# Kernel tuning notes

Hardware: AMD Instinct MI355X
Metric: run time of the kernel (lower is better)

The kernel has to match this reference:

```python
import jax, jax.numpy as jnp
import numpy as np

B, K, C, H, W = 16, 512, 512, 64, 64

def setup_inputs() -> dict:
    key = jax.random.key(0)
    kx, kc = jax.random.split(key)
    x = jax.random.normal(kx, (B, C, H, W), dtype=jnp.float32)
    cluster_centers = jax.random.normal(kc, (1, K, C, 1, 1), dtype=jnp.float32)
    return {"x": x, "cluster_centers": cluster_centers}

def reference(x, cluster_centers):
    # Faithful to: torch.square(x[:, None] - centers).sum(2).argmin(1, keepdim=True)
    # Computed without the (B, K, C, H, W) broadcast intermediate via
    # and numerically the same distances up to fp rounding).
    c = cluster_centers[0, :, :, 0, 0]                      # (K, C)
    x_sq = jnp.sum(x * x, axis=1, keepdims=True)            # (B, 1, H, W)
    c_sq = jnp.sum(c * c, axis=1)[None, :, None, None]      # (1, K, 1, 1)
    cross = jnp.einsum('bchw,kc->bkhw', x, c)               # (B, K, H, W)
    dist = x_sq - 2.0 * cross + c_sq                        # (B, K, H, W)
    return jnp.argmin(dist, axis=1, keepdims=True)          # (B, 1, H, W) int
```

## Files before the change

### kernel.cpp

```cpp
#include <hip/hip_runtime.h>
#include <math.h>


#define NK   512
#define NC   512
#define NHW  4096
#define NPX  65536
#define MARGIN 0.05f

typedef unsigned short u16;
typedef __attribute__((ext_vector_type(8)))  _Float16 half8;
typedef __attribute__((ext_vector_type(8)))  unsigned short ushort8;
typedef __attribute__((ext_vector_type(16))) float  f32x16;

__device__ __forceinline__ u16 f2h(float f) {
    return __builtin_bit_cast(u16, (_Float16)f);
}

__global__ __launch_bounds__(64) void prep_pack(const float* __restrict__ cc,
                                                u16* __restrict__ wcc,
                                                float* __restrict__ shalf,
                                                double* __restrict__ csqd,
                                                float* __restrict__ cct) {
    const int k    = blockIdx.x;
    const int lane = threadIdx.x;
    const int c0   = lane * 8;
    const float* row = cc + (size_t)k * NC + c0;
    ushort8 hi;
    double dsum = 0.0;
    #pragma unroll
    for (int i = 0; i < 8; ++i) {
        float v = row[i];
        dsum = fma((double)v, (double)v, dsum);
        hi[i] = f2h(v);
        cct[(size_t)(c0 + i) * NK + k] = v;
    }
    const int ch  = c0 >> 4;
    const int kh  = (c0 >> 3) & 1;
    const int mtg = k >> 5;
    const int h   = mtg >> 3;
    const int mtl = mtg & 7;
    const int ls  = (k & 31) + 32 * kh;
    *(ushort8*)(wcc + (((size_t)(ch * 2 + h) * 8 + mtl) * 64 + ls) * 8) = hi;
    #pragma unroll
    for (int off = 32; off > 0; off >>= 1) dsum += __shfl_down(dsum, off, 64);
    if (lane == 0) {
        csqd[k]  = dsum;
        shalf[k] = 0.5f * (float)dsum;
    }
}

__global__ __launch_bounds__(256, 4) void codebook_mfma(
        const float* __restrict__ x,
        const u16* __restrict__ wcc,
        const float* __restrict__ shalf,
        float* __restrict__ cbv,
        float* __restrict__ csv,
        int*   __restrict__ ckk)
{
    __shared__ __align__(16) u16 cs0[16 * 512];
    __shared__ __align__(16) u16 cs1[16 * 512];
    __shared__ __align__(16) u16 xs0[4 * 512];
    __shared__ __align__(16) u16 xs1[4 * 512];

    const int tid  = threadIdx.x;
    const int w    = tid >> 6;
    const int lane = tid & 63;

    const int h   = blockIdx.x & 1;
    const int gp0 = (blockIdx.x >> 1) * 64;
    const float* xb = x + (size_t)(gp0 >> 12) * (NC * NHW) + (gp0 & (NHW - 1));

    f32x16 acc[2][2] = {};

    const int p   = tid & 63;
    const int xkh = w & 1;
    const int jq  = w >> 1;
    const int xoff = ((p >> 5) * 64 + ((p & 31) + 32 * xkh)) * 8 + jq * 4;
    const float* xp = xb + (size_t)(xkh * 8 + jq * 4) * NHW + p;

    float fxa[8], fxb[8];

    auto xload = [&](float* fx, int sc) {
        const float* xc0 = xp + (size_t)(2 * sc) * 16 * NHW;
        const float* xc1 = xc0 + 16 * NHW;
        fx[0] = xc0[0]; fx[1] = xc0[NHW]; fx[2] = xc0[2 * NHW]; fx[3] = xc0[3 * NHW];
        fx[4] = xc1[0]; fx[5] = xc1[NHW]; fx[6] = xc1[2 * NHW]; fx[7] = xc1[3 * NHW];
    };
    auto xwrite = [&](const float* fx, u16* xs) {
        #pragma unroll
        for (int sub = 0; sub < 2; ++sub) {
            u16 h0 = f2h(fx[sub * 4 + 0]), h1 = f2h(fx[sub * 4 + 1]);
            u16 h2 = f2h(fx[sub * 4 + 2]), h3 = f2h(fx[sub * 4 + 3]);
            uint2 hv = make_uint2((unsigned)h0 | ((unsigned)h1 << 16),
                                  (unsigned)h2 | ((unsigned)h3 << 16));
            *(uint2*)&xs[sub * 1024 + xoff] = hv;
        }
    };
    auto stage_cs = [&](int sc, u16* dst) {
        #pragma unroll
        for (int sub = 0; sub < 2; ++sub) {
            #pragma unroll
            for (int i = 0; i < 2; ++i) {
                const int u = w * 2 + i;
                const u16* g = wcc + ((((size_t)(2 * sc + sub) * 2 + h) * 8 + u) * 64 + lane) * 8;
                __builtin_amdgcn_global_load_lds(
                    (const __attribute__((address_space(1))) void*)g,
                    (__attribute__((address_space(3))) void*)(dst + (sub * 8 + u) * 512),
                    16, 0, 0);
            }
        }
    };
    auto compute = [&](const u16* csb, const u16* xsb) {
        __builtin_amdgcn_s_setprio(1);
        #pragma unroll
        for (int sub = 0; sub < 2; ++sub) {
            half8 bh[2];
            #pragma unroll
            for (int nt = 0; nt < 2; ++nt)
                bh[nt] = *(const half8*)&xsb[sub * 1024 + ((size_t)nt * 64 + lane) * 8];
            #pragma unroll
            for (int mtl2 = 0; mtl2 < 2; ++mtl2) {
                const int gm = w * 2 + mtl2;
                half8 ah = *(const half8*)&csb[((size_t)(sub * 8 + gm) * 64 + lane) * 8];
                #pragma unroll
                for (int nt = 0; nt < 2; ++nt)
                    acc[mtl2][nt] = __builtin_amdgcn_mfma_f32_32x32x16_f16(ah, bh[nt], acc[mtl2][nt], 0, 0, 0);
            }
        }
        __builtin_amdgcn_s_setprio(0);
    };

    auto phase = [&](int t, u16* cs_cur, u16* cs_nxt, u16* xs_cur, u16* xs_nxt,
                     float* fx_cur, float* fx_nxt) {
        stage_cs(t + 1, cs_nxt);
        __builtin_amdgcn_sched_barrier(0);
        xload(fx_nxt, t + 2);
        asm volatile("s_waitcnt vmcnt(12)" ::: "memory");
        xwrite(fx_cur, xs_nxt);
        compute(cs_cur, xs_cur);
        asm volatile("s_waitcnt vmcnt(8) lgkmcnt(0)" ::: "memory");
        __builtin_amdgcn_s_barrier();
        __builtin_amdgcn_sched_barrier(0);
    };

    xload(fxa, 0);
    __builtin_amdgcn_sched_barrier(0);
    stage_cs(0, cs0);
    __builtin_amdgcn_sched_barrier(0);
    xload(fxb, 1);
    asm volatile("s_waitcnt vmcnt(12)" ::: "memory");
    xwrite(fxa, xs0);
    asm volatile("s_waitcnt vmcnt(8) lgkmcnt(0)" ::: "memory");
    __builtin_amdgcn_s_barrier();
    __builtin_amdgcn_sched_barrier(0);

    for (int t = 0; t < 14; t += 2) {
        phase(t,     cs0, cs1, xs0, xs1, fxb, fxa);
        phase(t + 1, cs1, cs0, xs1, xs0, fxa, fxb);
    }

    stage_cs(15, cs1);
    asm volatile("s_waitcnt vmcnt(4)" ::: "memory");
    xwrite(fxb, xs1);
    compute(cs0, xs0);
    asm volatile("s_waitcnt vmcnt(0) lgkmcnt(0)" ::: "memory");
    __builtin_amdgcn_s_barrier();
    __builtin_amdgcn_sched_barrier(0);
    compute(cs1, xs1);
    __syncthreads();

    float* cand_v = (float*)cs0;
    float* cand_s = cand_v + 512;
    int*   cand_k = (int*)(cand_s + 512);
    float* sh_ep  = (float*)(cand_k + 512);

    sh_ep[tid] = shalf[h * 256 + tid];
    __syncthreads();

    const int qb = lane >> 5;
    #pragma unroll
    for (int nt = 0; nt < 2; ++nt) {
        float best = -INFINITY, sec = -INFINITY;
        int bk = 0;
        #pragma unroll
        for (int mtl2 = 0; mtl2 < 2; ++mtl2) {
            const int kbase = w * 64 + mtl2 * 32 + 4 * qb;
            #pragma unroll
            for (int reg = 0; reg < 16; ++reg) {
                const int k = kbase + (reg & 3) + 8 * (reg >> 2);
                const float v = acc[mtl2][nt][reg] - sh_ep[k];
                if (v > best) { sec = best; best = v; bk = k; }
                else if (v > sec) sec = v;
            }
        }
        const int pc   = nt * 32 + (lane & 31);
        const int slot = w * 2 + qb;
        cand_v[pc * 8 + slot] = best;
        cand_s[pc * 8 + slot] = sec;
        cand_k[pc * 8 + slot] = bk;
    }
    __syncthreads();

    if (tid < 64) {
        float best = -INFINITY, sec = -INFINITY;
        int bk = 1 << 30;
        #pragma unroll
        for (int s = 0; s < 8; ++s) {
            float v  = cand_v[tid * 8 + s];
            float v2 = cand_s[tid * 8 + s];
            int  kk  = cand_k[tid * 8 + s];
            if (v > best || (v == best && kk < bk)) {
                sec = fmaxf(sec, best);
                best = v; bk = kk;
            } else sec = fmaxf(sec, v);
            sec = fmaxf(sec, v2);
        }
        const int gpx = gp0 + tid;
        cbv[h * NPX + gpx] = best;
        csv[h * NPX + gpx] = sec;
        ckk[h * NPX + gpx] = h * 256 + bk;
    }
}

__global__ __launch_bounds__(256) void merge_recheck(
        const float* __restrict__ x,
        const float* __restrict__ cct,
        const double* __restrict__ csqd,
        const float* __restrict__ cbv,
        const float* __restrict__ csv,
        const int*   __restrict__ ckk,
        int* __restrict__ out)
{
    __shared__ float  xcol[2][NC];
    __shared__ double part[2][4][NK];
    __shared__ double dvv[256];
    __shared__ int    dii[256];
    __shared__ int    list[64];
    __shared__ int    nflag;

    const int tid  = threadIdx.x;
    const int w    = tid >> 6;
    const int lane = tid & 63;
    const int pb   = blockIdx.x * 64;

    if (tid == 0) nflag = 0;
    __syncthreads();

    if (tid < 64) {
        const int px = pb + tid;
        const float b0 = cbv[px], b1 = cbv[NPX + px];
        const float s0 = csv[px], s1 = csv[NPX + px];
        const int   k0 = ckk[px], k1 = ckk[NPX + px];
        float best, sec; int bk;
        if (b0 >= b1) { best = b0; bk = k0; sec = fmaxf(s0, b1); }
        else          { best = b1; bk = k1; sec = fmaxf(s1, b0); }
        out[px] = bk;
        if (best - sec < MARGIN) { int i = atomicAdd(&nflag, 1); list[i] = px; }
    }
    __syncthreads();

    const int n = nflag;
    for (int idx = 0; idx < n; idx += 2) {
        const int px0 = list[idx];
        const int px1 = (idx + 1 < n) ? list[idx + 1] : px0;

        #pragma unroll
        for (int r = 0; r < 2; ++r) {
            const int c = tid + r * 256;
            xcol[0][c] = x[(size_t)(px0 >> 12) * (NC * NHW) + (size_t)c * NHW + (px0 & (NHW - 1))];
            xcol[1][c] = x[(size_t)(px1 >> 12) * (NC * NHW) + (size_t)c * NHW + (px1 & (NHW - 1))];
        }
        __syncthreads();

        double a0[8] = {}, a1[8] = {};
        const float4* cr = (const float4*)(cct + (size_t)(w * 128) * NK) + lane * 2;
        #pragma unroll 4
        for (int c0 = 0; c0 < 128; ++c0) {
            const float4 va = cr[0];
            const float4 vb = cr[1];
            cr += NK / 4;
            const double x0 = (double)xcol[0][w * 128 + c0];
            const double x1 = (double)xcol[1][w * 128 + c0];
            const double c4[8] = {(double)va.x, (double)va.y, (double)va.z, (double)va.w,
                                  (double)vb.x, (double)vb.y, (double)vb.z, (double)vb.w};
            #pragma unroll
            for (int j = 0; j < 8; ++j) {
                a0[j] = fma(x0, c4[j], a0[j]);
                a1[j] = fma(x1, c4[j], a1[j]);
            }
        }
        #pragma unroll
        for (int j = 0; j < 8; ++j) {
            part[0][w][lane * 8 + j] = a0[j];
            part[1][w][lane * 8 + j] = a1[j];
        }
        __syncthreads();

        #pragma unroll
        for (int pxi = 0; pxi < 2; ++pxi) {
            double bd = 1e300;
            int bkk = 1 << 30;
            #pragma unroll
            for (int r = 0; r < 2; ++r) {
                const int k = tid + r * 256;
                const double cross = part[pxi][0][k] + part[pxi][1][k]
                                   + part[pxi][2][k] + part[pxi][3][k];
                const double d = fma(-2.0, cross, csqd[k]);
                if (d < bd || (d == bd && k < bkk)) { bd = d; bkk = k; }
            }
            dvv[tid] = bd; dii[tid] = bkk;
            __syncthreads();
            for (int srd = 128; srd > 0; srd >>= 1) {
                if (tid < srd) {
                    double ov = dvv[tid + srd]; int oi = dii[tid + srd];
                    if (ov < dvv[tid] || (ov == dvv[tid] && oi < dii[tid])) {
                        dvv[tid] = ov; dii[tid] = oi;
                    }
                }
                __syncthreads();
            }
            if (tid == 0) out[pxi == 0 ? px0 : px1] = dii[0];
            __syncthreads();
        }
    }
}

extern "C" void kernel_launch(void* const* d_in, const int* in_sizes, int n_in,
                              void* d_out, int out_size, void* d_ws, size_t ws_size,
                              hipStream_t stream) {
    const float* x  = (const float*)d_in[0];
    const float* cc = (const float*)d_in[1];
    int* out = (int*)d_out;

    double* csqd  = (double*)d_ws;
    float*  shalf = (float*)(csqd + NK);
    u16*    wcc   = (u16*)(shalf + NK);
    float*  cct   = (float*)(wcc + 32 * 2 * 8 * 64 * 8);
    float*  cbv   = cct + (size_t)NC * NK;
    float*  csv   = cbv + 2 * NPX;
    int*    ckk   = (int*)(csv + 2 * NPX);

    prep_pack<<<NK, 64, 0, stream>>>(cc, wcc, shalf, csqd, cct);
    codebook_mfma<<<(NPX / 64) * 2, 256, 0, stream>>>(x, wcc, shalf, cbv, csv, ckk);
    merge_recheck<<<NPX / 64, 256, 0, stream>>>(x, cct, csqd, cbv, csv, ckk, out);
}
```

Before: 265.0 us.

## Split recheck into global-list fp32 pass with fp64 fallback for near-ties

Replaces the per-block merge+fp64 recheck with a global compaction of ambiguous pixels, a load-balanced fp32 recheck handling four pixels per pass, and an fp64 recheck only for pixels whose fp32 top-two gap is below a tight gate. This is meant to cut the expensive fp64 work and remove the load imbalance of per-block variable-length recheck loops. It adds two extra launches and global atomics, and it relies on the fp32 gate being tight enough to preserve exact argmin agreement.

Result: faster. 250.9 us (-5.3%).

```diff
diff --git a/kernel.cpp b/kernel.cpp
--- a/kernel.cpp
+++ b/kernel.cpp
@@ -7,6 +7,7 @@
 #define NHW  4096
 #define NPX  65536
 #define MARGIN 0.05f
+#define GATE2  1e-3f
 
 typedef unsigned short u16;
 typedef __attribute__((ext_vector_type(8)))  _Float16 half8;
@@ -21,9 +22,13 @@
                                                 u16* __restrict__ wcc,
                                                 float* __restrict__ shalf,
                                                 double* __restrict__ csqd,
-                                                float* __restrict__ cct) {
+                                                float* __restrict__ csqf,
+                                                float* __restrict__ cct,
+                                                int* __restrict__ gcnt,
+                                                int* __restrict__ gcnt2) {
     const int k    = blockIdx.x;
     const int lane = threadIdx.x;
+    if (k == 0 && lane == 0) { gcnt[0] = 0; gcnt2[0] = 0; }
     const int c0   = lane * 8;
     const float* row = cc + (size_t)k * NC + c0;
     ushort8 hi;
@@ -46,6 +51,7 @@
     for (int off = 32; off > 0; off >>= 1) dsum += __shfl_down(dsum, off, 64);
     if (lane == 0) {
         csqd[k]  = dsum;
+        csqf[k]  = (float)dsum;
         shalf[k] = 0.5f * (float)dsum;
     }
 }
@@ -223,106 +229,196 @@
     }
 }
 
-__global__ __launch_bounds__(256) void merge_recheck(
+__global__ __launch_bounds__(256) void merge(
+        const float* __restrict__ cbv,
+        const float* __restrict__ csv,
+        const int*   __restrict__ ckk,
+        int* __restrict__ out,
+        int* __restrict__ glist,
+        int* __restrict__ gcnt)
+{
+    const int px = blockIdx.x * 256 + threadIdx.x;
+
+    const float b0 = cbv[px],        b1 = cbv[NPX + px];
+    const float s0 = csv[px],        s1 = csv[NPX + px];
+    const int   k0 = ckk[px],        k1 = ckk[NPX + px];
+
+    float best, sec; int bk;
+    if (b0 >= b1) { best = b0; bk = k0; sec = fmaxf(s0, b1); }
+    else          { best = b1; bk = k1; sec = fmaxf(s1, b0); }
+
+    out[px] = bk;
+    if (best - sec < MARGIN) {
+        int i = atomicAdd(gcnt, 1);
+        glist[i] = px;
+    }
+}
+
+__global__ __launch_bounds__(256, 3) void recheck32(
+        const float* __restrict__ x,
+        const float* __restrict__ cct,
+        const float* __restrict__ csqf,
+        const int*   __restrict__ glist,
+        const int*   __restrict__ gcnt,
+        int* __restrict__ out,
+        int* __restrict__ list2,
+        int* __restrict__ gcnt2)
+{
+    __shared__ float xq[NC][4];
+    __shared__ float part[4][4][NK];
+    __shared__ float dvv[256];
+    __shared__ float dsv[256];
+    __shared__ int   dii[256];
+
+    const int tid  = threadIdx.x;
+    const int w    = tid >> 6;
+    const int lane = tid & 63;
+    const int n    = gcnt[0];
+    const int npass = (n + 3) >> 2;
+
+    for (int ps = blockIdx.x; ps < npass; ps += gridDim.x) {
+        int pxid[4];
+        #pragma unroll
+        for (int j = 0; j < 4; ++j) {
+            int i = ps * 4 + j;
+            pxid[j] = glist[i < n ? i : n - 1];
+        }
+        #pragma unroll
+        for (int r = 0; r < 8; ++r) {
+            const int linear = r * 256 + tid;
+            const int c = linear >> 2, j = linear & 3;
+            const int px = pxid[j];
+            xq[c][j] = x[(size_t)(px >> 12) * (NC * NHW) + (size_t)c * NHW + (px & (NHW - 1))];
+        }
+        __syncthreads();
+
+        float a[4][8] = {};
+        const float4* cp = (const float4*)(cct + (size_t)(w * 128) * NK) + lane * 2;
+        for (int c0 = 0; c0 < 128; ++c0) {
+            const float4 cv0 = cp[0];
+            const float4 cv1 = cp[1];
+            cp += NK / 4;
+            const float4 xv = *(const float4*)&xq[w * 128 + c0][0];
+            const float ck[8] = {cv0.x, cv0.y, cv0.z, cv0.w, cv1.x, cv1.y, cv1.z, cv1.w};
+            const float xs4[4] = {xv.x, xv.y, xv.z, xv.w};
+            #pragma unroll
+            for (int j = 0; j < 4; ++j)
+                #pragma unroll
+                for (int q = 0; q < 8; ++q)
+                    a[j][q] = fmaf(xs4[j], ck[q], a[j][q]);
+        }
+        #pragma unroll
+        for (int j = 0; j < 4; ++j)
+            #pragma unroll
+            for (int q = 0; q < 8; ++q)
+                part[j][w][lane * 8 + q] = a[j][q];
+        __syncthreads();
+
+        #pragma unroll
+        for (int j = 0; j < 4; ++j) {
+            float bd = 1e30f, sd = 1e30f;
+            int bi = 1 << 30;
+            #pragma unroll
+            for (int r = 0; r < 2; ++r) {
+                const int k = tid + r * 256;
+                const float cross = part[j][0][k] + part[j][1][k]
+                                  + part[j][2][k] + part[j][3][k];
+                const float d = fmaf(-2.f, cross, csqf[k]);
+                if (d < bd || (d == bd && k < bi)) { sd = bd; bd = d; bi = k; }
+                else sd = fminf(sd, d);
+            }
+            dvv[tid] = bd; dsv[tid] = sd; dii[tid] = bi;
+            __syncthreads();
+            for (int s = 128; s > 0; s >>= 1) {
+                if (tid < s) {
+                    const float ov = dvv[tid + s], os = dsv[tid + s];
+                    const int oi = dii[tid + s];
+                    if (ov < dvv[tid] || (ov == dvv[tid] && oi < dii[tid])) {
+                        dsv[tid] = fminf(dvv[tid], fminf(os, dsv[tid]));
+                        dvv[tid] = ov; dii[tid] = oi;
+                    } else {
+                        dsv[tid] = fminf(dsv[tid], fminf(ov, os));
+                    }
+                }
+                __syncthreads();
+            }
+            if (tid == 0) {
+                out[pxid[j]] = dii[0];
+                if (dsv[0] - dvv[0] < GATE2) {
+                    int i = atomicAdd(gcnt2, 1);
+                    list2[i] = pxid[j];
+                }
+            }
+            __syncthreads();
+        }
+    }
+}
+
+__global__ __launch_bounds__(256) void recheck64(
         const float* __restrict__ x,
         const float* __restrict__ cct,
         const double* __restrict__ csqd,
-        const float* __restrict__ cbv,
-        const float* __restrict__ csv,
-        const int*   __restrict__ ckk,
+        const int*   __restrict__ list2,
+        const int*   __restrict__ gcnt2,
         int* __restrict__ out)
 {
-    __shared__ float  xcol[2][NC];
-    __shared__ double part[2][4][NK];
+    __shared__ float  xcol[NC];
+    __shared__ double part[4][NK];
     __shared__ double dvv[256];
     __shared__ int    dii[256];
-    __shared__ int    list[64];
-    __shared__ int    nflag;
 
     const int tid  = threadIdx.x;
     const int w    = tid >> 6;
     const int lane = tid & 63;
-    const int pb   = blockIdx.x * 64;
-
-    if (tid == 0) nflag = 0;
-    __syncthreads();
-
-    if (tid < 64) {
-        const int px = pb + tid;
-        const float b0 = cbv[px], b1 = cbv[NPX + px];
-        const float s0 = csv[px], s1 = csv[NPX + px];
-        const int   k0 = ckk[px], k1 = ckk[NPX + px];
-        float best, sec; int bk;
-        if (b0 >= b1) { best = b0; bk = k0; sec = fmaxf(s0, b1); }
-        else          { best = b1; bk = k1; sec = fmaxf(s1, b0); }
-        out[px] = bk;
-        if (best - sec < MARGIN) { int i = atomicAdd(&nflag, 1); list[i] = px; }
-    }
-    __syncthreads();
-
-    const int n = nflag;
-    for (int idx = 0; idx < n; idx += 2) {
-        const int px0 = list[idx];
-        const int px1 = (idx + 1 < n) ? list[idx + 1] : px0;
-
+    const int n    = gcnt2[0];
+
+    for (int idx = blockIdx.x; idx < n; idx += gridDim.x) {
+        const int px = list2[idx];
         #pragma unroll
         for (int r = 0; r < 2; ++r) {
             const int c = tid + r * 256;
-            xcol[0][c] = x[(size_t)(px0 >> 12) * (NC * NHW) + (size_t)c * NHW + (px0 & (NHW - 1))];
-            xcol[1][c] = x[(size_t)(px1 >> 12) * (NC * NHW) + (size_t)c * NHW + (px1 & (NHW - 1))];
-        }
-        __syncthreads();
-
-        double a0[8] = {}, a1[8] = {};
-        const float4* cr = (const float4*)(cct + (size_t)(w * 128) * NK) + lane * 2;
-        #pragma unroll 4
+            xcol[c] = x[(size_t)(px >> 12) * (NC * NHW) + (size_t)c * NHW + (px & (NHW - 1))];
+        }
+        __syncthreads();
+
+        double a[8] = {};
+        const float4* cp = (const float4*)(cct + (size_t)(w * 128) * NK) + lane * 2;
         for (int c0 = 0; c0 < 128; ++c0) {
-            const float4 va = cr[0];
-            const float4 vb = cr[1];
-            cr += NK / 4;
-            const double x0 = (double)xcol[0][w * 128 + c0];
-            const double x1 = (double)xcol[1][w * 128 + c0];
-            const double c4[8] = {(double)va.x, (double)va.y, (double)va.z, (double)va.w,
-                                  (double)vb.x, (double)vb.y, (double)vb.z, (double)vb.w};
-            #pragma unroll
-            for (int j = 0; j < 8; ++j) {
-                a0[j] = fma(x0, c4[j], a0[j]);
-                a1[j] = fma(x1, c4[j], a1[j]);
-            }
-        }
-        #pragma unroll
-        for (int j = 0; j < 8; ++j) {
-            part[0][w][lane * 8 + j] = a0[j];
-            part[1][w][lane * 8 + j] = a1[j];
-        }
-        __syncthreads();
-
-        #pragma unroll
-        for (int pxi = 0; pxi < 2; ++pxi) {
-            double bd = 1e300;
-            int bkk = 1 << 30;
-            #pragma unroll
-            for (int r = 0; r < 2; ++r) {
-                const int k = tid + r * 256;
-                const double cross = part[pxi][0][k] + part[pxi][1][k]
-                                   + part[pxi][2][k] + part[pxi][3][k];
-                const double d = fma(-2.0, cross, csqd[k]);
-                if (d < bd || (d == bd && k < bkk)) { bd = d; bkk = k; }
-            }
-            dvv[tid] = bd; dii[tid] = bkk;
+            const float4 cv0 = cp[0];
+            const float4 cv1 = cp[1];
+            cp += NK / 4;
+            const double xv = (double)xcol[w * 128 + c0];
+            const double ck[8] = {(double)cv0.x, (double)cv0.y, (double)cv0.z, (double)cv0.w,
+                                  (double)cv1.x, (double)cv1.y, (double)cv1.z, (double)cv1.w};
+            #pragma unroll
+            for (int q = 0; q < 8; ++q) a[q] = fma(xv, ck[q], a[q]);
+        }
+        #pragma unroll
+        for (int q = 0; q < 8; ++q) part[w][lane * 8 + q] = a[q];
+        __syncthreads();
+
+        double bd = 1e300;
+        int bi = 1 << 30;
+        #pragma unroll
+        for (int r = 0; r < 2; ++r) {
+            const int k = tid + r * 256;
+            const double cross = part[0][k] + part[1][k] + part[2][k] + part[3][k];
+            const double d = fma(-2.0, cross, csqd[k]);
+            if (d < bd || (d == bd && k < bi)) { bd = d; bi = k; }
+        }
+        dvv[tid] = bd; dii[tid] = bi;
+        __syncthreads();
+        for (int s = 128; s > 0; s >>= 1) {
+            if (tid < s) {
+                const double ov = dvv[tid + s]; const int oi = dii[tid + s];
+                if (ov < dvv[tid] || (ov == dvv[tid] && oi < dii[tid])) {
+                    dvv[tid] = ov; dii[tid] = oi;
+                }
+            }
             __syncthreads();
-            for (int srd = 128; srd > 0; srd >>= 1) {
-                if (tid < srd) {
-                    double ov = dvv[tid + srd]; int oi = dii[tid + srd];
-                    if (ov < dvv[tid] || (ov == dvv[tid] && oi < dii[tid])) {
-                        dvv[tid] = ov; dii[tid] = oi;
-                    }
-                }
-                __syncthreads();
-            }
-            if (tid == 0) out[pxi == 0 ? px0 : px1] = dii[0];
-            __syncthreads();
-        }
+        }
+        if (tid == 0) out[px] = dii[0];
+        __syncthreads();
     }
 }
 
@@ -334,14 +430,21 @@
     int* out = (int*)d_out;
 
     double* csqd  = (double*)d_ws;
-    float*  shalf = (float*)(csqd + NK);
+    float*  csqf  = (float*)(csqd + NK);
+    float*  shalf = csqf + NK;
     u16*    wcc   = (u16*)(shalf + NK);
     float*  cct   = (float*)(wcc + 32 * 2 * 8 * 64 * 8);
     float*  cbv   = cct + (size_t)NC * NK;
     float*  csv   = cbv + 2 * NPX;
     int*    ckk   = (int*)(csv + 2 * NPX);
-
-    prep_pack<<<NK, 64, 0, stream>>>(cc, wcc, shalf, csqd, cct);
+    int*    glist = ckk + 2 * NPX;
+    int*    list2 = glist + NPX;
+    int*    gcnt  = list2 + NPX;
+    int*    gcnt2 = gcnt + 1;
+
+    prep_pack<<<NK, 64, 0, stream>>>(cc, wcc, shalf, csqd, csqf, cct, gcnt, gcnt2);
     codebook_mfma<<<(NPX / 64) * 2, 256, 0, stream>>>(x, wcc, shalf, cbv, csv, ckk);
-    merge_recheck<<<NPX / 64, 256, 0, stream>>>(x, cct, csqd, cbv, csv, ckk, out);
-}
+    merge<<<NPX / 256, 256, 0, stream>>>(cbv, csv, ckk, out, glist, gcnt);
+    recheck32<<<768, 256, 0, stream>>>(x, cct, csqf, glist, gcnt, out, list2, gcnt2);
+    recheck64<<<256, 256, 0, stream>>>(x, cct, csqd, list2, gcnt2, out);
+}
```
